# Kernel optimization log

Measured on AMD Instinct MI355X. Metric: run time of the kernel, lower is better.

The kernel has to match this reference:

```python
import jax, jax.numpy as jnp
import numpy as np

EPS_ATTN = 1e-5   # attention denominator eps (module eps)
EPS_LN = 1e-5     # nn.LayerNorm default eps


def _prime(x, proj):
    # Performer FAVOR+ hyperbolic positive features.
    # x: (B,H,L,dh), proj: (dh,m) -> (B,H,L,2m)
    dn = x.shape[-1] ** -0.25
    xn = dn * x
    d = jnp.einsum('bhld,dm->bhlm', xn, proj)
    diag = 0.5 * jnp.sum(xn * xn, axis=-1, keepdims=True)
    return jnp.concatenate([jnp.exp(d - diag), jnp.exp(-d - diag)], axis=-1)


def setup_inputs() -> dict:
    L, B, H, DH, DM, M = 2048, 4, 8, 64, 512, 256
    key = jax.random.key(0)
    k0, k1, k2 = jax.random.split(key, 3)
    h = jax.random.normal(k0, (L, B, DM), jnp.float32)
    w_qkv = jax.random.normal(k1, (H * 3 * DH, DM), jnp.float32) / np.sqrt(DM)
    w_o = jax.random.normal(k2, (DM, H * DH), jnp.float32) / np.sqrt(H * DH)
    ln_gamma = jnp.ones((DM,), jnp.float32)
    ln_beta = jnp.zeros((DM,), jnp.float32)
    # Gaussian orthogonal random matrix (blockwise QR), rows scaled by sqrt(dh)
    rng = np.random.default_rng(0)
    blocks = []
    for _ in range(M // DH):
        g = rng.standard_normal((DH, DH)).astype(np.float32)
        q, _ = np.linalg.qr(g)
        blocks.append(q.T)
    pm = np.concatenate(blocks, axis=0) * np.sqrt(DH)  # (M, DH)
    proj_matrix = jnp.asarray(pm.T.astype(np.float32))  # (DH, M)
    return {"h": h, "w_qkv": w_qkv, "w_o": w_o,
            "ln_gamma": ln_gamma, "ln_beta": ln_beta,
            "proj_matrix": proj_matrix}


def _forward(h, w_qkv, w_o, ln_gamma, ln_beta, proj_matrix):
    L, B, DM = h.shape
    DH, M = proj_matrix.shape
    H = w_qkv.shape[0] // (3 * DH)
    scale = DH ** -0.5

    qkv = (h @ w_qkv.T).reshape(L, B, H, 3 * DH)
    q, k, v = jnp.split(qkv, 3, axis=-1)
    q = jnp.transpose(q, (1, 2, 0, 3))  # (B,H,L,dh)
    k = jnp.transpose(k, (1, 2, 0, 3))
    v = jnp.transpose(v, (1, 2, 0, 3))

    qp = _prime(q, proj_matrix)  # (B,H,L,2M)
    kp = _prime(k, proj_matrix)
    kp = kp / jnp.sum(kp, axis=-1, keepdims=True)
    qp = qp / jnp.sum(qp, axis=-1, keepdims=True)

    den_acc = jnp.cumsum(kp, axis=2)
    denom = jnp.einsum('bhlm,bhlm->bhl', den_acc, qp)[..., None]  # (B,H,L,1)

    # fast_weight_sum: W_t = W_{t-1} + k_t v_t^T ; out_t = q_t @ W_t
    def step(W, xs):
        qt, kt, vt = xs  # (B,H,2M), (B,H,2M), (B,H,dh)
        W = W + kt[..., :, None] * vt[..., None, :]
        out = jnp.einsum('bhm,bhmd->bhd', qt, W)
        return W, out

    W0 = jnp.zeros((B, H, 2 * M, DH), h.dtype)
    xs = (jnp.transpose(qp, (2, 0, 1, 3)),
          jnp.transpose(kp, (2, 0, 1, 3)),
          jnp.transpose(v, (2, 0, 1, 3)))
    _, out = jax.lax.scan(step, W0, xs)  # (L,B,H,dh)
    out = jnp.transpose(out, (1, 2, 0, 3))  # (B,H,L,dh)

    out = scale * out / (denom + EPS_ATTN)
    out = jnp.transpose(out, (0, 2, 1, 3)).reshape(B, L, H * DH)  # (B,L,H*dh)
    out = jnp.swapaxes(out, 0, 1)  # (L,B,H*dh)

    attn_out = out @ w_o.T
    x = h + attn_out
    mu = jnp.mean(x, axis=-1, keepdims=True)
    var = jnp.mean((x - mu) ** 2, axis=-1, keepdims=True)
    return (x - mu) / jnp.sqrt(var + EPS_LN) * ln_gamma + ln_beta


def reference(h, w_qkv, w_o, ln_gamma, ln_beta, proj_matrix):
    return _forward(h, w_qkv, w_o, ln_gamma, ln_beta, proj_matrix)
```

## Files before the change

kernel.cpp:

```cpp
#include <hip/hip_runtime.h>
#include <hip/hip_fp16.h>
#include <math.h>

#define LSEQ 2048
#define NB 4
#define NH 8
#define DMID 512
#define CHK 128
#define SCALE 0.125f
#define DN 0.35355339059327373f
#define DN2 0.125f
#define LOG2E 1.4426950408889634f
#define EPS_ATTN 1e-5f
#define EPS_LN 1e-5f

typedef _Float16 f16x8 __attribute__((ext_vector_type(8)));
typedef _Float16 f16x4 __attribute__((ext_vector_type(4)));
typedef float f32x4 __attribute__((ext_vector_type(4)));

__device__ __forceinline__ float exp2a(float x) {
  float r;
  asm("v_exp_f32 %0, %1" : "=v"(r) : "v"(x));
  return r;
}

__device__ __forceinline__ void cvt16(const float* __restrict__ p,
                                      _Float16* __restrict__ dst) {
  float4 a = *(const float4*)p, b = *(const float4*)(p + 4);
  float4 c = *(const float4*)(p + 8), d = *(const float4*)(p + 12);
  f16x8 t0 = {(_Float16)a.x, (_Float16)a.y, (_Float16)a.z, (_Float16)a.w,
              (_Float16)b.x, (_Float16)b.y, (_Float16)b.z, (_Float16)b.w};
  f16x8 t1 = {(_Float16)c.x, (_Float16)c.y, (_Float16)c.z, (_Float16)c.w,
              (_Float16)d.x, (_Float16)d.y, (_Float16)d.z, (_Float16)d.w};
  *(f16x8*)dst = t0;
  *(f16x8*)(dst + 8) = t1;
}

__device__ __forceinline__ void cvt16r(const float4* __restrict__ r,
                                       _Float16* __restrict__ dst) {
  f16x8 t0 = {(_Float16)r[0].x, (_Float16)r[0].y, (_Float16)r[0].z,
              (_Float16)r[0].w, (_Float16)r[1].x, (_Float16)r[1].y,
              (_Float16)r[1].z, (_Float16)r[1].w};
  f16x8 t1 = {(_Float16)r[2].x, (_Float16)r[2].y, (_Float16)r[2].z,
              (_Float16)r[2].w, (_Float16)r[3].x, (_Float16)r[3].y,
              (_Float16)r[3].z, (_Float16)r[3].w};
  *(f16x8*)dst = t0;
  *(f16x8*)(dst + 8) = t1;
}

__device__ __forceinline__ void cvt8r(const float4* __restrict__ r,
                                      _Float16* __restrict__ dst) {
  f16x8 t0 = {(_Float16)r[0].x, (_Float16)r[0].y, (_Float16)r[0].z,
              (_Float16)r[0].w, (_Float16)r[1].x, (_Float16)r[1].y,
              (_Float16)r[1].z, (_Float16)r[1].w};
  *(f16x8*)dst = t0;
}

__global__ void k_diag(float* out, int n, float val) {
  int i = blockIdx.x * 256 + threadIdx.x;
  if (i < n) out[i] = val;
}

__global__ __launch_bounds__(256) void k_ptr(const float* __restrict__ proj,
                                             __half* __restrict__ projT) {
  int e = blockIdx.x * 256 + threadIdx.x;
  int n = e >> 6, k = e & 63;
  projT[e] = __float2half_rn(proj[k * 256 + n] * (DN * LOG2E));
}

__global__ __launch_bounds__(256) void k_qkv(
    const float* __restrict__ A, const float* __restrict__ Wq,
    __half* __restrict__ q, __half* __restrict__ k, __half* __restrict__ v) {
  __shared__ __align__(16) char smem[34816];
  _Float16* Ah = (_Float16*)smem;
  _Float16* Bh = (_Float16*)(smem + 10240);
  _Float16* Oh = (_Float16*)smem;

  const int tid = threadIdx.x;
  const int row0 = blockIdx.x * 128;
  const int col0 = blockIdx.y * 128;
  const int lane = tid & 63, wv = tid >> 6;
  const int ln15 = lane & 15, quad = lane >> 4;
  const int m0 = wv * 32;

  f32x4 Cacc[2][8];
  const f32x4 z4 = {0.f, 0.f, 0.f, 0.f};
#pragma unroll
  for (int mi = 0; mi < 2; ++mi)
#pragma unroll
    for (int nt = 0; nt < 8; ++nt) Cacc[mi][nt] = z4;

  const int srow = tid >> 1, sc = (tid & 1) * 16;
  const float* aptr = A + (size_t)(row0 + srow) * DMID + sc;
  const float* bptr = Wq + (size_t)(col0 + srow) * DMID + sc;

  float4 ra[4], rb[4];
#pragma unroll
  for (int i = 0; i < 4; ++i) {
    ra[i] = *(const float4*)(aptr + i * 4);
    rb[i] = *(const float4*)(bptr + i * 4);
  }

  for (int kt = 0; kt < DMID; kt += 32) {
    cvt16r(ra, &Ah[srow * 40 + sc]);
    cvt16r(rb, &Bh[srow * 40 + sc]);
    if (kt + 32 < DMID) {
#pragma unroll
      for (int i = 0; i < 4; ++i) {
        ra[i] = *(const float4*)(aptr + kt + 32 + i * 4);
        rb[i] = *(const float4*)(bptr + kt + 32 + i * 4);
      }
    }
    asm volatile("s_waitcnt lgkmcnt(0)" ::: "memory");
    __builtin_amdgcn_s_barrier();
    asm volatile("" ::: "memory");

    f16x8 a0 = *(const f16x8*)&Ah[(m0 + ln15) * 40 + quad * 8];
    f16x8 a1 = *(const f16x8*)&Ah[(m0 + 16 + ln15) * 40 + quad * 8];
#pragma unroll
    for (int nt = 0; nt < 8; ++nt) {
      f16x8 bf = *(const f16x8*)&Bh[(nt * 16 + ln15) * 40 + quad * 8];
      Cacc[0][nt] = __builtin_amdgcn_mfma_f32_16x16x32_f16(a0, bf, Cacc[0][nt], 0, 0, 0);
      Cacc[1][nt] = __builtin_amdgcn_mfma_f32_16x16x32_f16(a1, bf, Cacc[1][nt], 0, 0, 0);
    }
    asm volatile("" ::: "memory");
    __builtin_amdgcn_s_barrier();
    asm volatile("" ::: "memory");
  }
#pragma unroll
  for (int mi = 0; mi < 2; ++mi)
#pragma unroll
    for (int nt = 0; nt < 8; ++nt)
#pragma unroll
      for (int r = 0; r < 4; ++r)
        Oh[(m0 + mi * 16 + quad * 4 + r) * 136 + nt * 16 + ln15] =
            (_Float16)Cacc[mi][nt][r];
  __syncthreads();
  const int tr = tid >> 4, tc = tid & 15;
  const int col = col0 + tc * 8;
  const int hh = col / 192;
  const int rem = col - hh * 192;
  const int t = rem >> 6;
  const int d0 = rem & 63;
  __half* dstb = (t == 0) ? q : ((t == 1) ? k : v);
#pragma unroll
  for (int i = 0; i < 8; ++i) {
    int lrow = tr * 8 + i;
    int grow = row0 + lrow;
    int l = grow >> 2, bb = grow & 3;
    f16x8 val = *(const f16x8*)&Oh[lrow * 136 + tc * 8];
    *(f16x8*)((_Float16*)dstb + (((size_t)(bb * NH + hh) * LSEQ + l) << 6) + d0) = val;
  }
}

__global__ __launch_bounds__(512) void k_dgemm(
    const __half* __restrict__ qsrc, const __half* __restrict__ ksrc,
    const __half* __restrict__ projT, __half* __restrict__ dqd,
    __half* __restrict__ dkd, float* __restrict__ nq,
    float* __restrict__ nk) {
  __shared__ __align__(16) char smem[37888];
  _Float16* Bt = (_Float16*)smem;
  float* g_l  = (float*)(smem + 36864);
  float* ps_l = (float*)(smem + 37376);
  _Float16* Oh = (_Float16*)smem;

  const int tid = threadIdx.x;
  const __half* src = blockIdx.y ? ksrc : qsrc;
  __half* dst = blockIdx.y ? dkd : dqd;
  float* nrm = blockIdx.y ? nk : nq;
  const size_t r0 = (size_t)blockIdx.x * 128;

  const int lane = tid & 63, wv = tid >> 6;
  const int ln15 = lane & 15, quad = lane >> 4;
  const int m0 = wv * 16;

#pragma unroll
  for (int it = 0; it < 4; ++it) {
    int e = it * 512 + tid;
    int n = e >> 3, seg = e & 7;
    *(f16x8*)&Bt[n * 72 + seg * 8] =
        *(const f16x8*)((const _Float16*)projT + n * 64 + seg * 8);
  }

  f16x8 afrag[2];
  float ss = 0.f;
  {
    const _Float16* rp = (const _Float16*)src + (r0 + m0 + ln15) * 64;
#pragma unroll
    for (int ks = 0; ks < 2; ++ks) {
      f16x8 x8 = *(const f16x8*)(rp + ks * 32 + quad * 8);
      afrag[ks] = x8;
#pragma unroll
      for (int j = 0; j < 8; ++j) {
        float xv = (float)x8[j];
        ss = fmaf(xv, xv, ss);
      }
    }
    ss += __shfl_xor(ss, 16);
    ss += __shfl_xor(ss, 32);
  }
  if (quad == 0) g_l[m0 + ln15] = 0.5f * DN2 * LOG2E * ss;
  __syncthreads();

  f32x4 Cacc[16];
  const f32x4 z4 = {0.f, 0.f, 0.f, 0.f};
#pragma unroll
  for (int nt = 0; nt < 16; ++nt) Cacc[nt] = z4;

#pragma unroll
  for (int ks = 0; ks < 2; ++ks) {
    f16x8 a0 = afrag[ks];
#pragma unroll
    for (int nt = 0; nt < 16; ++nt) {
      f16x8 bf = *(const f16x8*)&Bt[(nt * 16 + ln15) * 72 + ks * 32 + quad * 8];
      Cacc[nt] = __builtin_amdgcn_mfma_f32_16x16x32_f16(a0, bf, Cacc[nt], 0, 0, 0);
    }
  }

  float gv[4], pp[4];
#pragma unroll
  for (int r = 0; r < 4; ++r) {
    gv[r] = g_l[m0 + quad * 4 + r];
    pp[r] = 0.f;
  }
#pragma unroll
  for (int nt = 0; nt < 16; ++nt)
#pragma unroll
    for (int r = 0; r < 4; ++r) {
      float d = Cacc[nt][r];
      pp[r] += exp2a(d - gv[r]) + exp2a(-d - gv[r]);
    }
#pragma unroll
  for (int r = 0; r < 4; ++r) {
    float p = pp[r];
    p += __shfl_xor(p, 1); p += __shfl_xor(p, 2);
    p += __shfl_xor(p, 4); p += __shfl_xor(p, 8);
    if (ln15 == 0) ps_l[m0 + quad * 4 + r] = p;
  }

#pragma unroll
  for (int hf = 0; hf < 2; ++hf) {
    __syncthreads();
#pragma unroll
    for (int nt2 = 0; nt2 < 8; ++nt2) {
      int nt = hf * 8 + nt2;
#pragma unroll
      for (int r = 0; r < 4; ++r)
        Oh[(m0 + quad * 4 + r) * 136 + nt2 * 16 + ln15] =
            (_Float16)Cacc[nt][r];
    }
    __syncthreads();
#pragma unroll
    for (int it = 0; it < 4; ++it) {
      int e = it * 512 + tid;
      int row = e >> 4, seg = e & 15;
      *(f16x8*)((_Float16*)dst + (r0 + row) * 256 + hf * 128 + seg * 8) =
          *(const f16x8*)&Oh[row * 136 + seg * 8];
    }
  }
  if (tid < 128) nrm[r0 + tid] = g_l[tid] + __log2f(ps_l[tid]);
}

__global__ __launch_bounds__(512) void k_kv(
    const __half* __restrict__ dk, const float* __restrict__ nk,
    const __half* __restrict__ v, __half* __restrict__ KVt,
    float* __restrict__ Ks) {
  __shared__ __align__(16) char smem[52736];
  _Float16* kpT = (_Float16*)smem;
  _Float16* Vt  = (_Float16*)(smem + 34816);
  float* ck = (float*)(smem + 52224);
  _Float16* Oh2 = (_Float16*)smem;

  const int tid = threadIdx.x;
  const int cidx = blockIdx.x;
  const size_t rowbase = (size_t)cidx * CHK;
  const int lane = tid & 63, wv = tid >> 6;
  const int ln15 = lane & 15, quad = lane >> 4;

  if (tid < 128) ck[tid] = nk[rowbase + tid];
  {
    int s = tid & 127, dq0 = (tid >> 7) * 16;
    const _Float16* vsrc = (const _Float16*)v + (rowbase + s) * 64 + dq0;
    f16x8 v0 = ((const f16x8*)vsrc)[0];
    f16x8 v1 = ((const f16x8*)vsrc)[1];
#pragma unroll
    for (int j = 0; j < 8; ++j) {
      Vt[(dq0 + j) * 136 + s] = v0[j];
      Vt[(dq0 + 8 + j) * 136 + s] = v1[j];
    }
  }

  const int srow = tid >> 2;
  const int scol = (tid & 3) * 32;

  f16x8 bone;
#pragma unroll
  for (int j = 0; j < 8; ++j)
    bone[j] = (ln15 == 0) ? (_Float16)1.0f : (_Float16)0.0f;

  bool first = true;
#pragma unroll
  for (int cp = 0; cp < 2; ++cp) {
    f16x8 rk[4];
    const _Float16* dsrc =
        (const _Float16*)dk + (rowbase + srow) * 256 + cp * 128 + scol;
#pragma unroll
    for (int it = 0; it < 4; ++it) rk[it] = *(const f16x8*)(dsrc + it * 8);
    float c = ck[srow];
    if (first) { __syncthreads(); c = ck[srow]; }

#pragma unroll
    for (int sg = 0; sg < 2; ++sg) {
      const int i0 = sg * 256 + cp * 128;
      const float fsign = sg ? -1.f : 1.f;
      if (!first) __syncthreads();
      first = false;
#pragma unroll
      for (int it = 0; it < 4; ++it) {
        f16x8 d8 = rk[it];
#pragma unroll
        for (int j = 0; j < 8; ++j)
          kpT[(scol + it * 8 + j) * 136 + srow] =
              (_Float16)exp2a(fmaf((float)d8[j], fsign, -c));
      }
      __syncthreads();

      f32x4 Cacc[4], Kacc;
      const f32x4 z4 = {0.f, 0.f, 0.f, 0.f};
#pragma unroll
      for (int nt = 0; nt < 4; ++nt) Cacc[nt] = z4;
      Kacc = z4;
#pragma unroll
      for (int ks = 0; ks < 4; ++ks) {
        f16x8 a0 = *(const f16x8*)&kpT[(wv * 16 + ln15) * 136 + ks * 32 + quad * 8];
#pragma unroll
        for (int nt = 0; nt < 4; ++nt) {
          f16x8 bV = *(const f16x8*)&Vt[(nt * 16 + ln15) * 136 + ks * 32 + quad * 8];
          Cacc[nt] = __builtin_amdgcn_mfma_f32_16x16x32_f16(a0, bV, Cacc[nt], 0, 0, 0);
        }
        Kacc = __builtin_amdgcn_mfma_f32_16x16x32_f16(a0, bone, Kacc, 0, 0, 0);
      }
      if (ln15 == 0) {
#pragma unroll
        for (int r = 0; r < 4; ++r)
          Ks[(size_t)cidx * 512 + i0 + wv * 16 + quad * 4 + r] = Kacc[r];
      }
      __syncthreads();

#pragma unroll
      for (int nt = 0; nt < 4; ++nt) {
        f16x4 pack = {(_Float16)Cacc[nt][0], (_Float16)Cacc[nt][1],
                      (_Float16)Cacc[nt][2], (_Float16)Cacc[nt][3]};
        *(f16x4*)&Oh2[(nt * 16 + ln15) * 136 + wv * 16 + quad * 4] = pack;
      }
      __syncthreads();
      {
        int d = tid >> 3, part = tid & 7;
        _Float16* dstp =
            (_Float16*)KVt + (size_t)cidx * 32768 + d * 512 + i0 + part * 16;
        const _Float16* srcp = &Oh2[d * 136 + part * 16];
        *(f16x8*)(dstp) = *(const f16x8*)(srcp);
        *(f16x8*)(dstp + 8) = *(const f16x8*)(srcp + 8);
      }
    }
  }
}

__global__ __launch_bounds__(256) void k_scan(__half2* __restrict__ KV2,
                                              float* __restrict__ Ks) {
  const int bh = blockIdx.x;
  const int tid = threadIdx.x;
  if (blockIdx.y < 32) {
    uint2* p = (uint2*)(KV2 + (size_t)bh * 262144) + (blockIdx.y * 256 + tid);
    uint2 raw[16];
#pragma unroll
    for (int c = 0; c < 16; ++c) raw[c] = p[c * 8192];
    float ax0 = 0.f, ay0 = 0.f, ax1 = 0.f, ay1 = 0.f;
#pragma unroll
    for (int c = 0; c < 16; ++c) {
      __half2 h0 = *(__half2*)&raw[c].x;
      __half2 h1 = *(__half2*)&raw[c].y;
      float2 f0 = __half22float2(h0), f1 = __half22float2(h1);
      __half2 o0 = __floats2half2_rn(ax0, ay0);
      __half2 o1 = __floats2half2_rn(ax1, ay1);
      uint2 o;
      o.x = *(unsigned*)&o0;
      o.y = *(unsigned*)&o1;
      p[c * 8192] = o;
      ax0 += f0.x; ay0 += f0.y; ax1 += f1.x; ay1 += f1.y;
    }
  } else {
    int i = (blockIdx.y - 32) * 256 + tid;
    float* pk = Ks + (size_t)bh * 8192 + i;
    float vs[16];
#pragma unroll
    for (int c = 0; c < 16; ++c) vs[c] = pk[c * 512];
    float a = 0.f;
#pragma unroll
    for (int c = 0; c < 16; ++c) { pk[c * 512] = a; a += vs[c]; }
  }
}

__global__ __launch_bounds__(512) void k_attn(
    const __half* __restrict__ dq, const __half* __restrict__ dk,
    const float* __restrict__ nq, const float* __restrict__ nk,
    const __half* __restrict__ v, const __half* __restrict__ KVt,
    const float* __restrict__ Kpre, float* __restrict__ outb) {
  __shared__ __align__(16) char smem[53760];
  _Float16* qpT = (_Float16*)(smem);
  _Float16* kpT = (_Float16*)(smem + 18432);
  _Float16* WT  = (_Float16*)(smem + 36864);
  float*    KpT = (float*)(smem + 46080);
  float* cq_l   = (float*)(smem + 46336);
  float* ck_l   = (float*)(smem + 46848);
  _Float16* S_h = (_Float16*)(smem);
  _Float16* Vt  = (_Float16*)(smem + 34816);
  float* den1_l = (float*)(smem + 52224);
  float* den2_l = (float*)(smem + 52736);
  float* invd_l = (float*)(smem + 53248);

  const int tid = threadIdx.x;
  const int cidx = blockIdx.x;
  const int cc = cidx & 15, bh = cidx >> 4;
  const size_t rowb = (size_t)cidx * 128;
  const int lane = tid & 63;
  const int wv = tid >> 6;
  const int H = wv >> 2;
  const int m0 = (wv & 3) * 16;
  const int ln15 = lane & 15, quad = lane >> 4;

  if (tid < 128) cq_l[tid] = nq[rowb + tid];
  else if (tid < 256) ck_l[tid - 128] = nk[rowb + tid - 128];
  __syncthreads();

  const int c8 = tid & 7;
  const int r9 = tid >> 3;
  const int csrc = (c8 & 3) * 8;
  const float sgnf = (c8 < 4) ? 1.f : -1.f;

  const _Float16* qsrc = (const _Float16*)dq + (rowb + r9) * 256 + csrc;
  const _Float16* ksrc = (const _Float16*)dk + (rowb + r9) * 256 + csrc;
  const _Float16* wsrc = (const _Float16*)KVt + (size_t)cidx * 32768 +
                         r9 * 512 + ((c8 < 4) ? 0 : 256) + csrc;
  const float* kpsrc = Kpre + (size_t)cidx * 512 +
                       ((tid < 32) ? tid : (tid < 64 ? 224 + tid : 0));

  float cq[2], ck2[2];
#pragma unroll
  for (int p = 0; p < 2; ++p) {
    cq[p] = cq_l[r9 + p * 64];
    ck2[p] = ck_l[r9 + p * 64];
  }

  f16x8 rq[2], rk[2];
#pragma unroll
  for (int p = 0; p < 2; ++p) {
    rq[p] = *(const f16x8*)(qsrc + p * 16384);
    rk[p] = *(const f16x8*)(ksrc + p * 16384);
  }
  f16x8 wcur = *(const f16x8*)(wsrc);
  float kpcur = kpsrc[0];

  f32x4 Sacc[8], Oacc[4], Dacc;
  const f32x4 z4 = {0.f, 0.f, 0.f, 0.f};
#pragma unroll
  for (int nt = 0; nt < 8; ++nt) Sacc[nt] = z4;
#pragma unroll
  for (int nt = 0; nt < 4; ++nt) Oacc[nt] = z4;
  Dacc = z4;

  const int NSw = H ? 8 : 4;

  for (int it = 0; it < 8; ++it) {
    const int kb = it * 32;
    f16x8 wnxt;
    float kpnxt = 0.f;
    if (it < 7) {
      wnxt = *(const f16x8*)(wsrc + kb + 32);
      kpnxt = kpsrc[kb + 32];
    }

#pragma unroll
    for (int p = 0; p < 2; ++p) {
      f16x8 d = rq[p], t;
#pragma unroll
      for (int j = 0; j < 8; ++j)
        t[j] = (_Float16)exp2a(fmaf((float)d[j], sgnf, -cq[p]));
      *(f16x8*)&qpT[(r9 + p * 64) * 72 + c8 * 8] = t;
    }
#pragma unroll
    for (int p = 0; p < 2; ++p) {
      f16x8 d = rk[p], t;
#pragma unroll
      for (int j = 0; j < 8; ++j)
        t[j] = (_Float16)exp2a(fmaf((float)d[j], sgnf, -ck2[p]));
      *(f16x8*)&kpT[(r9 + p * 64) * 72 + c8 * 8] = t;
    }

    if (it < 7) {
#pragma unroll
      for (int p = 0; p < 2; ++p) {
        rq[p] = *(const f16x8*)(qsrc + p * 16384 + kb + 32);
        rk[p] = *(const f16x8*)(ksrc + p * 16384 + kb + 32);
      }
    }
    *(f16x8*)&WT[r9 * 72 + c8 * 8] = wcur;
    if (tid < 64) KpT[tid] = kpcur;

    asm volatile("s_waitcnt lgkmcnt(0)" ::: "memory");
    __builtin_amdgcn_s_barrier();
    asm volatile("" ::: "memory");

    __builtin_amdgcn_s_setprio(1);
#pragma unroll
    for (int ks = 0; ks < 2; ++ks) {
      f16x8 a0 = *(const f16x8*)&qpT[(H * 64 + m0 + ln15) * 72 + ks * 32 + quad * 8];
#pragma unroll
      for (int nt = 0; nt < 4; ++nt) {
        f16x8 bf = *(const f16x8*)&kpT[(nt * 16 + ln15) * 72 + ks * 32 + quad * 8];
        Sacc[nt] = __builtin_amdgcn_mfma_f32_16x16x32_f16(a0, bf, Sacc[nt], 0, 0, 0);
      }
      if (H) {
#pragma unroll
        for (int nt = 4; nt < 8; ++nt) {
          f16x8 bf = *(const f16x8*)&kpT[(nt * 16 + ln15) * 72 + ks * 32 + quad * 8];
          Sacc[nt] = __builtin_amdgcn_mfma_f32_16x16x32_f16(a0, bf, Sacc[nt], 0, 0, 0);
        }
      }
#pragma unroll
      for (int nt = 0; nt < 4; ++nt) {
        f16x8 bw = *(const f16x8*)&WT[(nt * 16 + ln15) * 72 + ks * 32 + quad * 8];
        Oacc[nt] = __builtin_amdgcn_mfma_f32_16x16x32_f16(a0, bw, Oacc[nt], 0, 0, 0);
      }
      f16x8 bk;
#pragma unroll
      for (int j = 0; j < 8; ++j)
        bk[j] = (ln15 == 0) ? (_Float16)KpT[ks * 32 + quad * 8 + j]
                            : (_Float16)0.f;
      Dacc = __builtin_amdgcn_mfma_f32_16x16x32_f16(a0, bk, Dacc, 0, 0, 0);
    }
    __builtin_amdgcn_s_setprio(0);

    asm volatile("" ::: "memory");
    __builtin_amdgcn_s_barrier();
    asm volatile("" ::: "memory");

    if (it < 7) { wcur = wnxt; kpcur = kpnxt; }
  }

  if (ln15 == 0) {
#pragma unroll
    for (int r = 0; r < 4; ++r)
      den2_l[H * 64 + m0 + quad * 4 + r] = Dacc[r];
  }
  {
    _Float16* S_me = S_h + H * 8704;
    float dp[4] = {0.f, 0.f, 0.f, 0.f};
#pragma unroll
    for (int nt = 0; nt < 8; ++nt) {
      if (nt < NSw) {
        int s = nt * 16 + ln15;
#pragma unroll
        for (int r = 0; r < 4; ++r) {
          int tl = m0 + quad * 4 + r;
          float vsv = (s <= H * 64 + tl) ? Sacc[nt][r] : 0.f;
          dp[r] += vsv;
          S_me[tl * 136 + s] = (_Float16)vsv;
        }
      }
    }
#pragma unroll
    for (int r = 0; r < 4; ++r) {
      float p = dp[r];
      p += __shfl_xor(p, 1); p += __shfl_xor(p, 2);
      p += __shfl_xor(p, 4); p += __shfl_xor(p, 8);
      if (ln15 == 0) den1_l[H * 64 + m0 + quad * 4 + r] = p;
    }
  }
  {
    int s = tid & 127, d0v = (tid >> 7) * 16;
    const _Float16* vsrc = (const _Float16*)v + (rowb + s) * 64 + d0v;
    f16x8 v0 = ((const f16x8*)vsrc)[0];
    f16x8 v1 = ((const f16x8*)vsrc)[1];
#pragma unroll
    for (int j = 0; j < 8; ++j) {
      Vt[(d0v + j) * 136 + s] = v0[j];
      Vt[(d0v + 8 + j) * 136 + s] = v1[j];
    }
  }
  __syncthreads();
  if (tid < 128)
    invd_l[tid] = SCALE / (den1_l[tid] + den2_l[tid] + EPS_ATTN);
  __syncthreads();
  {
    _Float16* S_me = S_h + H * 8704;
#pragma unroll
    for (int ks = 0; ks < 4; ++ks) {
      if (ks < (H ? 4 : 2)) {
        f16x8 aS0 = *(const f16x8*)&S_me[(m0 + ln15) * 136 + ks * 32 + quad * 8];
#pragma unroll
        for (int nt = 0; nt < 4; ++nt) {
          f16x8 bV = *(const f16x8*)&Vt[(nt * 16 + ln15) * 136 + ks * 32 + quad * 8];
          Oacc[nt] = __builtin_amdgcn_mfma_f32_16x16x32_f16(aS0, bV, Oacc[nt], 0, 0, 0);
        }
      }
    }
  }
  const int b = bh >> 3, hh = bh & 7;
  float ivv[4];
#pragma unroll
  for (int r = 0; r < 4; ++r)
    ivv[r] = invd_l[H * 64 + m0 + quad * 4 + r];
#pragma unroll
  for (int nt = 0; nt < 4; ++nt) {
    int dcol = nt * 16 + ln15;
#pragma unroll
    for (int r = 0; r < 4; ++r) {
      int l = cc * 128 + H * 64 + m0 + quad * 4 + r;
      outb[((size_t)l * 4 + b) * 512 + hh * 64 + dcol] = Oacc[nt][r] * ivv[r];
    }
  }
}

__global__ __launch_bounds__(256) void k_oproj(
    const float* __restrict__ A, const float* __restrict__ Wo,
    const float* __restrict__ hres, float* __restrict__ xout) {
  __shared__ __align__(16) char smem[17408];
  _Float16* Ah = (_Float16*)smem;
  _Float16* Bh = (_Float16*)(smem + 5120);
  _Float16* Oh = (_Float16*)smem;

  const int tid = threadIdx.x;
  const int row0 = blockIdx.x * 64;
  const int col0 = blockIdx.y * 128;
  const int lane = tid & 63, wv = tid >> 6;
  const int ln15 = lane & 15, quad = lane >> 4;
  const int m0 = wv * 16;

  f32x4 Cacc[8];
  const f32x4 z4 = {0.f, 0.f, 0.f, 0.f};
#pragma unroll
  for (int nt = 0; nt < 8; ++nt) Cacc[nt] = z4;

  const int arow = tid >> 2, asc = (tid & 3) * 8;
  const int brow = tid >> 1, bsc = (tid & 1) * 16;
  const float* aptr = A + (size_t)(row0 + arow) * DMID + asc;
  const float* bptr = Wo + (size_t)(col0 + brow) * DMID + bsc;

  float4 ra[2], rb[4];
#pragma unroll
  for (int i = 0; i < 2; ++i) ra[i] = *(const float4*)(aptr + i * 4);
#pragma unroll
  for (int i = 0; i < 4; ++i) rb[i] = *(const float4*)(bptr + i * 4);

  for (int kt = 0; kt < DMID; kt += 32) {
    cvt8r(ra, &Ah[arow * 40 + asc]);
    cvt16r(rb, &Bh[brow * 40 + bsc]);
    if (kt + 32 < DMID) {
#pragma unroll
      for (int i = 0; i < 2; ++i)
        ra[i] = *(const float4*)(aptr + kt + 32 + i * 4);
#pragma unroll
      for (int i = 0; i < 4; ++i)
        rb[i] = *(const float4*)(bptr + kt + 32 + i * 4);
    }
    asm volatile("s_waitcnt lgkmcnt(0)" ::: "memory");
    __builtin_amdgcn_s_barrier();
    asm volatile("" ::: "memory");

    f16x8 a0 = *(const f16x8*)&Ah[(m0 + ln15) * 40 + quad * 8];
#pragma unroll
    for (int nt = 0; nt < 8; ++nt) {
      f16x8 bf = *(const f16x8*)&Bh[(nt * 16 + ln15) * 40 + quad * 8];
      Cacc[nt] = __builtin_amdgcn_mfma_f32_16x16x32_f16(a0, bf, Cacc[nt], 0, 0, 0);
    }
    asm volatile("" ::: "memory");
    __builtin_amdgcn_s_barrier();
    asm volatile("" ::: "memory");
  }
#pragma unroll
  for (int nt = 0; nt < 8; ++nt)
#pragma unroll
    for (int r = 0; r < 4; ++r)
      Oh[(m0 + quad * 4 + r) * 136 + nt * 16 + ln15] = (_Float16)Cacc[nt][r];
  __syncthreads();
  const int tr = tid >> 4, tc = tid & 15;
#pragma unroll
  for (int i = 0; i < 4; ++i) {
    int lrow = tr * 4 + i;
    int grow = row0 + lrow;
    size_t base = (size_t)grow * 512 + col0 + tc * 8;
    f16x8 o = *(const f16x8*)&Oh[lrow * 136 + tc * 8];
    float4 h0 = *(const float4*)(hres + base);
    float4 h1 = *(const float4*)(hres + base + 4);
    *(float4*)(xout + base) =
        make_float4((float)o[0] + h0.x, (float)o[1] + h0.y,
                    (float)o[2] + h0.z, (float)o[3] + h0.w);
    *(float4*)(xout + base + 4) =
        make_float4((float)o[4] + h1.x, (float)o[5] + h1.y,
                    (float)o[6] + h1.z, (float)o[7] + h1.w);
  }
}

__global__ __launch_bounds__(256) void k_ln(float* __restrict__ x,
                                            const float* __restrict__ g,
                                            const float* __restrict__ bta) {
  __shared__ float ws_[4], wq_[4];
  const int row = blockIdx.x;
  const int tid = threadIdx.x;
  float2 vv = *(const float2*)(x + (size_t)row * 512 + tid * 2);
  float s = vv.x + vv.y;
  float sq = vv.x * vv.x + vv.y * vv.y;
#pragma unroll
  for (int off = 1; off < 64; off <<= 1) {
    s += __shfl_xor(s, off, 64);
    sq += __shfl_xor(sq, off, 64);
  }
  if ((tid & 63) == 0) { ws_[tid >> 6] = s; wq_[tid >> 6] = sq; }
  __syncthreads();
  s = ws_[0] + ws_[1] + ws_[2] + ws_[3];
  sq = wq_[0] + wq_[1] + wq_[2] + wq_[3];
  float mu = s * (1.f / 512.f);
  float var = sq * (1.f / 512.f) - mu * mu;
  float rstd = rsqrtf(var + EPS_LN);
  int c = tid * 2;
  float2 o;
  o.x = (vv.x - mu) * rstd * g[c] + bta[c];
  o.y = (vv.y - mu) * rstd * g[c + 1] + bta[c + 1];
  *(float2*)(x + (size_t)row * 512 + c) = o;
}

extern "C" void kernel_launch(void* const* d_in, const int* in_sizes, int n_in,
                              void* d_out, int out_size, void* d_ws,
                              size_t ws_size, hipStream_t stream) {
  const float* h    = (const float*)d_in[0];
  const float* wqkv = (const float*)d_in[1];
  const float* wo   = (const float*)d_in[2];
  const float* g    = (const float*)d_in[3];
  const float* bta  = (const float*)d_in[4];
  const float* proj = (const float*)d_in[5];
  float* out = (float*)d_out;
  char* wsb = (char*)d_ws;

  __half* q   = (__half*)(wsb + 0);
  __half* kb  = (__half*)(wsb + 8388608);
  __half* vb  = (__half*)(wsb + 16777216);
  __half* dq  = (__half*)(wsb + 25165824);
  __half* dk  = (__half*)(wsb + 58720256);
  float*  nq  = (float*)(wsb + 92274688);
  float*  nk  = (float*)(wsb + 92798976);
  __half* KVt = (__half*)(wsb + 93323264);
  float*  Ks  = (float*)(wsb + 126877696);
  __half* pT  = (__half*)(wsb + 127926272);
  float* outb = (float*)(wsb + 0);

  if (ws_size < 127959040ull) {
    float val = 1000.0f + (float)(ws_size >> 20);
    k_diag<<<(out_size + 255) / 256, 256, 0, stream>>>(out, out_size, val);
    return;
  }

  k_ptr  <<<dim3(64), 256, 0, stream>>>(proj, pT);
  k_qkv  <<<dim3(64, 12), 256, 0, stream>>>(h, wqkv, q, kb, vb);
  k_dgemm<<<dim3(512, 2), 512, 0, stream>>>(q, kb, pT, dq, dk, nq, nk);
  k_kv   <<<dim3(512), 512, 0, stream>>>(dk, nk, vb, KVt, Ks);
  k_scan <<<dim3(32, 34), 256, 0, stream>>>((__half2*)KVt, Ks);
  k_attn <<<dim3(512), 512, 0, stream>>>(dq, dk, nq, nk, vb, KVt, Ks, outb);
  k_oproj<<<dim3(128, 4), 256, 0, stream>>>(outb, wo, h, out);
  k_ln   <<<dim3(8192), 256, 0, stream>>>(out, g, bta);
}
```

Baseline: 226.5 us.

## Enlarge QKV GEMM tile to 256 rows with 512 threads per block

```diff
diff --git a/kernel.cpp b/kernel.cpp
--- a/kernel.cpp
+++ b/kernel.cpp
@@ -68,16 +68,16 @@
   projT[e] = __float2half_rn(proj[k * 256 + n] * (DN * LOG2E));
 }
 
-__global__ __launch_bounds__(256) void k_qkv(
+__global__ __launch_bounds__(512) void k_qkv(
     const float* __restrict__ A, const float* __restrict__ Wq,
     __half* __restrict__ q, __half* __restrict__ k, __half* __restrict__ v) {
   __shared__ __align__(16) char smem[34816];
   _Float16* Ah = (_Float16*)smem;
-  _Float16* Bh = (_Float16*)(smem + 10240);
+  _Float16* Bh = (_Float16*)(smem + 20480);
   _Float16* Oh = (_Float16*)smem;
 
   const int tid = threadIdx.x;
-  const int row0 = blockIdx.x * 128;
+  const int row0 = blockIdx.x * 256;
   const int col0 = blockIdx.y * 128;
   const int lane = tid & 63, wv = tid >> 6;
   const int ln15 = lane & 15, quad = lane >> 4;
@@ -90,25 +90,29 @@
 #pragma unroll
     for (int nt = 0; nt < 8; ++nt) Cacc[mi][nt] = z4;
 
-  const int srow = tid >> 1, sc = (tid & 1) * 16;
-  const float* aptr = A + (size_t)(row0 + srow) * DMID + sc;
-  const float* bptr = Wq + (size_t)(col0 + srow) * DMID + sc;
+  const int sarow = tid >> 1, sac = (tid & 1) * 16;
+  const float* aptr = A + (size_t)(row0 + sarow) * DMID + sac;
+  const float* bptr = Wq + (size_t)(col0 + sarow) * DMID + sac;
 
   float4 ra[4], rb[4];
 #pragma unroll
-  for (int i = 0; i < 4; ++i) {
-    ra[i] = *(const float4*)(aptr + i * 4);
-    rb[i] = *(const float4*)(bptr + i * 4);
+  for (int i = 0; i < 4; ++i) ra[i] = *(const float4*)(aptr + i * 4);
+  if (tid < 256) {
+#pragma unroll
+    for (int i = 0; i < 4; ++i) rb[i] = *(const float4*)(bptr + i * 4);
   }
 
   for (int kt = 0; kt < DMID; kt += 32) {
-    cvt16r(ra, &Ah[srow * 40 + sc]);
-    cvt16r(rb, &Bh[srow * 40 + sc]);
+    cvt16r(ra, &Ah[sarow * 40 + sac]);
+    if (tid < 256) cvt16r(rb, &Bh[sarow * 40 + sac]);
     if (kt + 32 < DMID) {
 #pragma unroll
-      for (int i = 0; i < 4; ++i) {
+      for (int i = 0; i < 4; ++i)
         ra[i] = *(const float4*)(aptr + kt + 32 + i * 4);
-        rb[i] = *(const float4*)(bptr + kt + 32 + i * 4);
+      if (tid < 256) {
+#pragma unroll
+        for (int i = 0; i < 4; ++i)
+          rb[i] = *(const float4*)(bptr + kt + 32 + i * 4);
       }
     }
     asm volatile("s_waitcnt lgkmcnt(0)" ::: "memory");
@@ -127,15 +131,7 @@
     __builtin_amdgcn_s_barrier();
     asm volatile("" ::: "memory");
   }
-#pragma unroll
-  for (int mi = 0; mi < 2; ++mi)
-#pragma unroll
-    for (int nt = 0; nt < 8; ++nt)
-#pragma unroll
-      for (int r = 0; r < 4; ++r)
-        Oh[(m0 + mi * 16 + quad * 4 + r) * 136 + nt * 16 + ln15] =
-            (_Float16)Cacc[mi][nt][r];
-  __syncthreads();
+
   const int tr = tid >> 4, tc = tid & 15;
   const int col = col0 + tc * 8;
   const int hh = col / 192;
@@ -143,13 +139,30 @@
   const int t = rem >> 6;
   const int d0 = rem & 63;
   __half* dstb = (t == 0) ? q : ((t == 1) ? k : v);
-#pragma unroll
-  for (int i = 0; i < 8; ++i) {
-    int lrow = tr * 8 + i;
-    int grow = row0 + lrow;
-    int l = grow >> 2, bb = grow & 3;
-    f16x8 val = *(const f16x8*)&Oh[lrow * 136 + tc * 8];
-    *(f16x8*)((_Float16*)dstb + (((size_t)(bb * NH + hh) * LSEQ + l) << 6) + d0) = val;
+
+#pragma unroll
+  for (int hf = 0; hf < 2; ++hf) {
+    if ((wv >> 2) == hf) {
+      int lm = (wv & 3) * 32;
+#pragma unroll
+      for (int mi = 0; mi < 2; ++mi)
+#pragma unroll
+        for (int nt = 0; nt < 8; ++nt)
+#pragma unroll
+          for (int r = 0; r < 4; ++r)
+            Oh[(lm + mi * 16 + quad * 4 + r) * 136 + nt * 16 + ln15] =
+                (_Float16)Cacc[mi][nt][r];
+    }
+    __syncthreads();
+#pragma unroll
+    for (int i = 0; i < 4; ++i) {
+      int lrow = tr * 4 + i;
+      int grow = row0 + hf * 128 + lrow;
+      int l = grow >> 2, bb = grow & 3;
+      f16x8 val = *(const f16x8*)&Oh[lrow * 136 + tc * 8];
+      *(f16x8*)((_Float16*)dstb + (((size_t)(bb * NH + hh) * LSEQ + l) << 6) + d0) = val;
+    }
+    __syncthreads();
   }
 }
 
@@ -761,7 +774,7 @@
   }
 
   k_ptr  <<<dim3(64), 256, 0, stream>>>(proj, pT);
-  k_qkv  <<<dim3(64, 12), 256, 0, stream>>>(h, wqkv, q, kb, vb);
+  k_qkv  <<<dim3(32, 12), 512, 0, stream>>>(h, wqkv, q, kb, vb);
   k_dgemm<<<dim3(512, 2), 512, 0, stream>>>(q, kb, pT, dq, dk, nq, nk);
   k_kv   <<<dim3(512), 512, 0, stream>>>(dk, nk, vb, KVt, Ks);
   k_scan <<<dim3(32, 34), 256, 0, stream>>>((__half2*)KVt, Ks);
```

Result: no change. 223.4 us, median of 2 (-1.3%).
